# Kernel optimization log

Hardware: AMD Instinct MI355X
Metric: run time of the kernel (lower is better)

## Reference

```python
import jax, jax.numpy as jnp
import numpy as np

EPS_BN = 1e-5

def _l2n(v, axis):
    return v / jnp.maximum(jnp.linalg.norm(v, axis=axis, keepdims=True), 1e-12)

def _bn_relu(x, g, b):
    # x: [B, C, K]; BatchNorm2d training-mode stats over (B, K) per channel, then ReLU
    m = x.mean(axis=(0, 2), keepdims=True)
    v = x.var(axis=(0, 2), keepdims=True)
    return jax.nn.relu(g[None, :, None] * (x - m) * jax.lax.rsqrt(v + EPS_BN) + b[None, :, None])

def _conv_bn_relu(x, W, g, b):
    # 1x1 conv (no bias) == channel matmul
    return _bn_relu(jnp.einsum('oi,bik->bok', W, x), g, b)

def _graphnet(x, anchor, sigma_p):
    # NetVLAD-style soft assignment; vectorized over clusters (no [B,K,N,C] intermediate)
    B, C, H, W = x.shape
    N = H * W
    sig = jax.nn.sigmoid(sigma_p)                              # [K, C]
    xf = x.reshape(B, C, N).transpose(0, 2, 1)                 # [B, N, C]
    inv_s2 = 1.0 / (sig * sig)                                 # [K, C]
    q = (jnp.einsum('bnc,kc->bnk', xf * xf, inv_s2)
         - 2.0 * jnp.einsum('bnc,kc->bnk', xf, anchor * inv_s2)
         + jnp.sum(anchor * anchor * inv_s2, axis=-1))         # [B, N, K]
    assign = jax.nn.softmax(-0.5 * q.transpose(0, 2, 1), axis=1)  # [B, K, N], softmax over clusters
    s = assign.sum(axis=-1)                                    # [B, K]
    wx = jnp.einsum('bkn,bnc->bkc', assign, xf)                # [B, K, C]
    nodes = (wx - s[..., None] * anchor[None]) / sig[None] / (s[..., None] + 1e-9)
    nodes = _l2n(nodes, 2)
    flat = _l2n(nodes.reshape(B, -1), 1)
    # faithful to torch: flat view as (B, C, K) is a pure reshape of [B, K, C] data
    return flat.reshape(B, C, anchor.shape[0]), assign

def _cascade_gcn(x, W1, W2):
    # loop=2 cascaded GCN: adj = softmax(x^T x), out = (adj @ (x^T W))^T
    for Wg in (W1, W2):
        adj = jax.nn.softmax(jnp.einsum('bik,bil->bkl', x, x), axis=2)   # [B, K, K]
        sup = jnp.einsum('bik,io->bko', x, Wg)                           # [B, K, C]
        x = jnp.einsum('bkl,blo->bok', adj, sup)                         # [B, C, K]
    return jax.nn.relu(x)

def _mutual(edge, r1, r2, assign, g1, g2, cw, cg, cb):
    # cross-graph correlation + cascade GCN + project back to pixels
    a = jax.nn.softmax(jnp.einsum('bik,bil->bkl', edge, r1), axis=-1)    # [B, K, K]
    m = jnp.einsum('bkl,bcl->bck', a, r2)                                # [B, C, K]
    edge = _cascade_gcn(edge + m, g1, g2)
    ex = jnp.einsum('bck,bkn->bcn', edge, assign)                        # [B, C, N]
    return _conv_bn_relu(ex, cw, cg, cb)


def setup_inputs() -> dict:
    key = jax.random.key(0)
    B, C, H, W, K = 16, 256, 64, 64, 8
    ks = jax.random.split(key, 40)
    sc = 1.0 / np.sqrt(C)
    d = {
        'rgb':   jax.random.normal(ks[0], (B, C, H, W), jnp.float32),
        't':     jax.random.normal(ks[1], (B, C, H, W), jnp.float32),
        'edger': jax.random.normal(ks[2], (B, C, H, W), jnp.float32),
        'edget': jax.random.normal(ks[3], (B, C, H, W), jnp.float32),
        'pred_w': jax.random.normal(ks[4], (1, C), jnp.float32) * sc,
        'pred_b': jax.random.normal(ks[5], (1,), jnp.float32) * 0.1,
        'rgb_anchor': jax.random.uniform(ks[6], (K, C), jnp.float32),
        'rgb_sigma':  jax.random.uniform(ks[7], (K, C), jnp.float32),
        't_anchor':   jax.random.uniform(ks[8], (K, C), jnp.float32),
        't_sigma':    jax.random.uniform(ks[9], (K, C), jnp.float32),
    }
    i = 10
    for name in ['rgb_c1', 'rgb_c2', 't_c1', 't_c2', 't2r_conv', 'r2t_conv']:
        d[name + '_w'] = jax.random.normal(ks[i], (C, C), jnp.float32) * sc; i += 1
        d[name + '_g'] = jax.random.uniform(ks[i], (C,), jnp.float32); i += 1
        d[name + '_b'] = jnp.zeros((C,), jnp.float32)
    for name in ['t2r_g1', 't2r_g2', 'r2t_g1', 'r2t_g2']:
        d[name + '_w'] = jax.random.normal(ks[i], (C, C), jnp.float32) * sc; i += 1
    return d


def reference(rgb, t, edger, edget, pred_w, pred_b,
              rgb_anchor, rgb_sigma, t_anchor, t_sigma,
              rgb_c1_w, rgb_c1_g, rgb_c1_b, rgb_c2_w, rgb_c2_g, rgb_c2_b,
              t_c1_w, t_c1_g, t_c1_b, t_c2_w, t_c2_g, t_c2_b,
              t2r_conv_w, t2r_conv_g, t2r_conv_b,
              r2t_conv_w, r2t_conv_g, r2t_conv_b,
              t2r_g1_w, t2r_g2_w, r2t_g1_w, r2t_g2_w):
    # edge-gated features
    edge_r = jnp.einsum('oi,bihw->bohw', pred_w, edger) + pred_b.reshape(1, -1, 1, 1)
    rgb_x = jax.nn.sigmoid(edge_r) * rgb
    edge_t = jnp.einsum('oi,bihw->bohw', pred_w, edget) + pred_b.reshape(1, -1, 1, 1)
    t_x = jax.nn.sigmoid(edge_t) * t
    # graph projection
    rgb_graph, rgb_assign = _graphnet(rgb_x, rgb_anchor, rgb_sigma)
    t_graph, t_assign = _graphnet(t_x, t_anchor, t_sigma)
    rgb_g1 = _conv_bn_relu(rgb_graph, rgb_c1_w, rgb_c1_g, rgb_c1_b)
    rgb_g2 = _conv_bn_relu(rgb_graph, rgb_c2_w, rgb_c2_g, rgb_c2_b)
    t_g1 = _conv_bn_relu(t_graph, t_c1_w, t_c1_g, t_c1_b)
    t_g2 = _conv_bn_relu(t_graph, t_c2_w, t_c2_g, t_c2_b)
    # mutual graph interaction
    n_rgb = _mutual(rgb_graph, t_g1, t_g2, rgb_assign, t2r_g1_w, t2r_g2_w,
                    t2r_conv_w, t2r_conv_g, t2r_conv_b)
    rgb_x = rgb_x + n_rgb.reshape(rgb_x.shape)
    n_t = _mutual(t_graph, rgb_g1, rgb_g2, t_assign, r2t_g1_w, r2t_g2_w,
                  r2t_conv_w, r2t_conv_g, r2t_conv_b)
    t_x = t_x + n_t.reshape(t_x.shape)
    return (rgb_x, t_x)
```

## Files before the change

kernel.cpp:

```cpp
#include <hip/hip_runtime.h>
#include <math.h>

#define BB 16
#define CC 256
#define NN 4096
#define KK 8

#define OFF_S      ((size_t)0)
#define OFF_WX     ((size_t)256)
#define OFF_G      ((size_t)65792)
#define OFF_CS     ((size_t)67840)
#define OFF_MS     ((size_t)69888)
#define OFF_CK     ((size_t)70912)
#define ACC_FLOATS ((size_t)70928)
#define OFF_ASSIGN ((size_t)70928)
#define OFF_GRAPH  ((size_t)1119504)
#define OFF_CLP    ((size_t)1185040)
#define OFF_WT     ((size_t)1193232)
#define OFF_Y      ((size_t)1586448)
#define OFF_CE     ((size_t)1717520)
#define WS_FLOATS  ((size_t)1783056)

__global__ __launch_bounds__(256) void k0_prep(
    const float* __restrict__ w0, const float* __restrict__ w1,
    const float* __restrict__ w2, const float* __restrict__ w3,
    const float* __restrict__ w4, const float* __restrict__ w5,
    const float* __restrict__ anch_r, const float* __restrict__ sig_r,
    const float* __restrict__ anch_t, const float* __restrict__ sig_t,
    float* __restrict__ ws)
{
    int bid = blockIdx.x, tid = threadIdx.x;
    if (bid < 1536) {
        int widx = bid >> 8;
        int e = ((bid & 255) << 8) + tid;
        int o = e >> 8, i = e & 255;
        const float* W = widx == 0 ? w0 : widx == 1 ? w1 : widx == 2 ? w2 :
                         widx == 3 ? w3 : widx == 4 ? w4 : w5;
        ws[OFF_WT + (size_t)widx * 65536 + (size_t)i * 256 + o] = W[o * 256 + i];
    } else {
        int pid = ((bid - 1536) << 8) + tid;
        int M = pid >> 11, j = pid & 2047;
        int k = j >> 8, c = j & 255;
        const float* sg = M ? sig_t : sig_r;
        const float* an = M ? anch_t : anch_r;
        float s = 1.f / (1.f + expf(-sg[j]));
        float is2 = 1.f / (s * s);
        float a = an[j];
        float2* c2 = (float2*)(ws + OFF_CLP);
        c2[(size_t)M * 2048 + (size_t)c * 8 + k] = make_float2(is2, -2.f * a * is2);
        atomicAdd(&ws[OFF_CK + (size_t)M * 8 + k], a * a * is2);
    }
}

__global__ __launch_bounds__(256) void k1_gate_assign(
    const float* __restrict__ rgb, const float* __restrict__ t,
    const float* __restrict__ edger, const float* __restrict__ edget,
    const float* __restrict__ pred_w, const float* __restrict__ pred_b,
    float* __restrict__ out, float* __restrict__ ws)
{
    int tile = blockIdx.x;
    int b    = blockIdx.y;
    int M    = blockIdx.z;
    int tid  = threadIdx.x;
    int tx = tid & 63, ty = tid >> 6;
    int n0 = tile * 64;

    const float* X = M ? t : rgb;
    const float* E = M ? edget : edger;

    __shared__ _Float16 xs[CC][66];
    __shared__ float qp[KK][4][64];
    __shared__ float gatep[4][64];
    __shared__ float gate_s[64];
    __shared__ float asg[KK][64];
    __shared__ float cks[KK];

    if (tid < KK) cks[tid] = ws[OFF_CK + (size_t)M * 8 + tid];

    const float* Eb = E + ((size_t)b * CC) * NN + n0 + tx;
    float acc = 0.f;
#pragma unroll 4
    for (int c = ty * 64; c < ty * 64 + 64; ++c)
        acc += pred_w[c] * Eb[(size_t)c * NN];
    gatep[ty][tx] = acc;
    __syncthreads();
    if (tid < 64) {
        float g = gatep[0][tx] + gatep[1][tx] + gatep[2][tx] + gatep[3][tx] + pred_b[0];
        float sg = 1.f / (1.f + expf(-g));
        gate_s[tx] = sg;
        out[(((size_t)M * BB + b) * CC) * NN + n0 + tx] = sg;
    }
    __syncthreads();

    const float* Xb = X + ((size_t)b * CC) * NN + n0 + tx;
    const float4* prq = (const float4*)(ws + OFF_CLP) + (size_t)M * 1024;
    float gt = gate_s[tx];
    float qk[KK];
#pragma unroll
    for (int k = 0; k < KK; ++k) qk[k] = 0.f;
#pragma unroll 2
    for (int c = ty * 64; c < ty * 64 + 64; ++c) {
        float x = gt * Xb[(size_t)c * NN];
        xs[c][tx] = (_Float16)x;
        float xx = x * x;
        float4 p0 = prq[c * 4 + 0];
        float4 p1 = prq[c * 4 + 1];
        float4 p2 = prq[c * 4 + 2];
        float4 p3 = prq[c * 4 + 3];
        qk[0] += xx * p0.x + x * p0.y;  qk[1] += xx * p0.z + x * p0.w;
        qk[2] += xx * p1.x + x * p1.y;  qk[3] += xx * p1.z + x * p1.w;
        qk[4] += xx * p2.x + x * p2.y;  qk[5] += xx * p2.z + x * p2.w;
        qk[6] += xx * p3.x + x * p3.y;  qk[7] += xx * p3.z + x * p3.w;
    }
#pragma unroll
    for (int k = 0; k < KK; ++k) qp[k][ty][tx] = qk[k];
    __syncthreads();

    float* assign_g = ws + OFF_ASSIGN + (((size_t)M * BB + b) * KK) * NN;
    if (tid < 64) {
        float q[KK], mx = -1e30f;
#pragma unroll
        for (int k = 0; k < KK; ++k) {
            q[k] = -0.5f * (qp[k][0][tx] + qp[k][1][tx] + qp[k][2][tx] + qp[k][3][tx] + cks[k]);
            mx = fmaxf(mx, q[k]);
        }
        float sm = 0.f;
#pragma unroll
        for (int k = 0; k < KK; ++k) { q[k] = expf(q[k] - mx); sm += q[k]; }
        float inv = 1.f / sm;
#pragma unroll
        for (int k = 0; k < KK; ++k) {
            float a = q[k] * inv;
            asg[k][tx] = a;
            assign_g[(size_t)k * NN + n0 + tx] = a;
        }
    }
    __syncthreads();

    {
        int c = tid;
        float a0[KK];
#pragma unroll
        for (int k = 0; k < KK; ++k) a0[k] = 0.f;
#pragma unroll 4
        for (int j = 0; j < 64; ++j) {
            float xv = (float)xs[c][j];
#pragma unroll
            for (int k = 0; k < KK; ++k) a0[k] += asg[k][j] * xv;
        }
        float* wx_g = ws + OFF_WX + ((size_t)M * BB + b) * KK * CC;
#pragma unroll
        for (int k = 0; k < KK; ++k)
            atomicAdd(&wx_g[k * CC + c], a0[k]);
    }
    if (tid < 64) {
        int k1 = tid >> 3, k2 = tid & 7;
        float g = 0.f;
        for (int j = 0; j < 64; ++j) g += asg[k1][j] * asg[k2][j];
        atomicAdd(&ws[OFF_G + ((size_t)M * BB + b) * 64 + tid], g);
    } else if (tid < 72) {
        int k = tid - 64;
        float sv = 0.f;
        for (int j = 0; j < 64; ++j) sv += asg[k][j];
        atomicAdd(&ws[OFF_S + ((size_t)M * BB + b) * KK + k], sv);
    }
}

__global__ __launch_bounds__(256) void k2_nodes(
    const float* __restrict__ anch_r, const float* __restrict__ sig_r,
    const float* __restrict__ anch_t, const float* __restrict__ sig_t,
    float* __restrict__ ws)
{
    int b = blockIdx.x & 15, M = blockIdx.x >> 4;
    int c = threadIdx.x;
    const float* an = M ? anch_t : anch_r;
    const float* sg = M ? sig_t : sig_r;
    const float* wx = ws + OFF_WX + ((size_t)M * BB + b) * KK * CC;
    const float* sp = ws + OFF_S + ((size_t)M * BB + b) * KK;
    float* gout = ws + OFF_GRAPH + ((size_t)M * BB + b) * 2048;

    __shared__ float nod[KK][CC];
    __shared__ float nrm[KK];
    __shared__ float gp[CC];
    __shared__ float gnrm;

    float node[KK];
#pragma unroll
    for (int k = 0; k < KK; ++k) {
        float s = sp[k];
        float sig = 1.f / (1.f + expf(-sg[k * CC + c]));
        float v = (wx[k * CC + c] - s * an[k * CC + c]) / sig / (s + 1e-9f);
        node[k] = v;
        nod[k][c] = v;
    }
    __syncthreads();
    if (c < KK) {
        float ss = 0.f;
        for (int i = 0; i < CC; ++i) ss += nod[c][i] * nod[c][i];
        nrm[c] = fmaxf(sqrtf(ss), 1e-12f);
    }
    __syncthreads();
    float gs = 0.f;
#pragma unroll
    for (int k = 0; k < KK; ++k) { node[k] /= nrm[k]; gs += node[k] * node[k]; }
    gp[c] = gs;
    __syncthreads();
    if (c == 0) {
        float ss = 0.f;
        for (int i = 0; i < CC; ++i) ss += gp[i];
        gnrm = fmaxf(sqrtf(ss), 1e-12f);
    }
    __syncthreads();
    float inv = 1.f / gnrm;
#pragma unroll
    for (int k = 0; k < KK; ++k)
        gout[k * CC + c] = node[k] * inv;
}

__global__ __launch_bounds__(256) void k3_conv(float* __restrict__ ws)
{
    int conv = blockIdx.x >> 4, b = blockIdx.x & 15;
    int o = threadIdx.x;
    int M = conv >> 1;
    const float* gsrc = ws + OFF_GRAPH + ((size_t)M * BB + b) * 2048;
    const float* wt = ws + OFF_WT + (size_t)conv * 65536;
    __shared__ float gsh[2048];
    for (int i = o; i < 2048; i += 256) gsh[i] = gsrc[i];
    __syncthreads();
    float acc[KK];
#pragma unroll
    for (int k = 0; k < KK; ++k) acc[k] = 0.f;
    for (int i = 0; i < CC; ++i) {
        float w = wt[(size_t)i * 256 + o];
#pragma unroll
        for (int k = 0; k < KK; ++k) acc[k] += w * gsh[i * 8 + k];
    }
    float* y = ws + OFF_Y + ((size_t)conv * BB + b) * 2048;
    float s1 = 0.f, s2 = 0.f;
#pragma unroll
    for (int k = 0; k < KK; ++k) { y[o * 8 + k] = acc[k]; s1 += acc[k]; s2 += acc[k] * acc[k]; }
    atomicAdd(&ws[OFF_CS + (size_t)conv * 512 + o], s1);
    atomicAdd(&ws[OFF_CS + (size_t)conv * 512 + 256 + o], s2);
}

__device__ __forceinline__ void gcn_layer(const float* __restrict__ Wg,
                                          float* xin, float* xout, float* am,
                                          float* sup, int o, bool do_relu)
{
    if (o < 64) {
        int k = o >> 3, l = o & 7;
        float s = 0.f;
        for (int i = 0; i < CC; ++i) s += xin[i * 9 + k] * xin[i * 9 + l];
        am[k * 9 + l] = s;
    }
    __syncthreads();
    if (o < 8) {
        float mx = -1e30f;
#pragma unroll
        for (int l = 0; l < 8; ++l) mx = fmaxf(mx, am[o * 9 + l]);
        float e[8], sm = 0.f;
#pragma unroll
        for (int l = 0; l < 8; ++l) { e[l] = expf(am[o * 9 + l] - mx); sm += e[l]; }
        float inv = 1.f / sm;
#pragma unroll
        for (int l = 0; l < 8; ++l) am[o * 9 + l] = e[l] * inv;
    }
    float sa[8];
#pragma unroll
    for (int k = 0; k < 8; ++k) sa[k] = 0.f;
    for (int i = 0; i < CC; ++i) {
        float w = Wg[(size_t)i * 256 + o];
#pragma unroll
        for (int k = 0; k < 8; ++k) sa[k] += xin[i * 9 + k] * w;
    }
#pragma unroll
    for (int k = 0; k < 8; ++k) sup[k * 256 + o] = sa[k];
    __syncthreads();
#pragma unroll
    for (int k = 0; k < 8; ++k) {
        float v = 0.f;
#pragma unroll
        for (int l = 0; l < 8; ++l) v += am[k * 9 + l] * sup[l * 256 + o];
        xout[o * 9 + k] = do_relu ? fmaxf(v, 0.f) : v;
    }
    __syncthreads();
}

__global__ __launch_bounds__(256) void k4_mutual(
    const float* __restrict__ rc1g, const float* __restrict__ rc1b,
    const float* __restrict__ rc2g, const float* __restrict__ rc2b,
    const float* __restrict__ tc1g, const float* __restrict__ tc1b,
    const float* __restrict__ tc2g, const float* __restrict__ tc2b,
    const float* __restrict__ t2rg1, const float* __restrict__ t2rg2,
    const float* __restrict__ r2tg1, const float* __restrict__ r2tg2,
    float* __restrict__ ws)
{
    int D = blockIdx.x >> 4, b = blockIdx.x & 15;
    int o = threadIdx.x;
    int M = D;
    int convR1 = D ? 0 : 2;
    int convR2 = D ? 1 : 3;
    const float* g1p = D ? rc1g : tc1g;  const float* b1p = D ? rc1b : tc1b;
    const float* g2p = D ? rc2g : tc2g;  const float* b2p = D ? rc2b : tc2b;
    const float* gcn1 = D ? r2tg1 : t2rg1;
    const float* gcn2 = D ? r2tg2 : t2rg2;
    const float* cwT = ws + OFF_WT + (size_t)(4 + D) * 65536;

    __shared__ float edge_s[CC * 9];
    __shared__ float r1_s[CC * 9];
    __shared__ float r2_s[CC * 9];
    __shared__ float x0[CC * 9];
    __shared__ float x1[CC * 9];
    __shared__ float sup[KK * CC];
    __shared__ float am[KK * 9];
    __shared__ float sS[KK];
    __shared__ float gS[64];

    if (o < 8)  sS[o] = ws[OFF_S + ((size_t)M * BB + b) * 8 + o];
    if (o < 64) gS[o] = ws[OFF_G + ((size_t)M * BB + b) * 64 + o];

    const float* egr = ws + OFF_GRAPH + ((size_t)M * BB + b) * 2048;
    const float* y1 = ws + OFF_Y + ((size_t)convR1 * BB + b) * 2048;
    const float* y2 = ws + OFF_Y + ((size_t)convR2 * BB + b) * 2048;
    float m1 = ws[OFF_CS + (size_t)convR1 * 512 + o] * (1.f / 128.f);
    float q1 = ws[OFF_CS + (size_t)convR1 * 512 + 256 + o] * (1.f / 128.f);
    float al1 = g1p[o] * rsqrtf(q1 - m1 * m1 + 1e-5f);
    float be1 = b1p[o] - m1 * al1;
    float m2 = ws[OFF_CS + (size_t)convR2 * 512 + o] * (1.f / 128.f);
    float q2 = ws[OFF_CS + (size_t)convR2 * 512 + 256 + o] * (1.f / 128.f);
    float al2 = g2p[o] * rsqrtf(q2 - m2 * m2 + 1e-5f);
    float be2 = b2p[o] - m2 * al2;
#pragma unroll
    for (int k = 0; k < 8; ++k) {
        edge_s[o * 9 + k] = egr[o * 8 + k];
        r1_s[o * 9 + k] = fmaxf(al1 * y1[o * 8 + k] + be1, 0.f);
        r2_s[o * 9 + k] = fmaxf(al2 * y2[o * 8 + k] + be2, 0.f);
    }
    __syncthreads();

    if (o < 64) {
        int k = o >> 3, l = o & 7;
        float s = 0.f;
        for (int i = 0; i < CC; ++i) s += edge_s[i * 9 + k] * r1_s[i * 9 + l];
        am[k * 9 + l] = s;
    }
    __syncthreads();
    if (o < 8) {
        float mx = -1e30f;
#pragma unroll
        for (int l = 0; l < 8; ++l) mx = fmaxf(mx, am[o * 9 + l]);
        float e[8], sm = 0.f;
#pragma unroll
        for (int l = 0; l < 8; ++l) { e[l] = expf(am[o * 9 + l] - mx); sm += e[l]; }
        float inv = 1.f / sm;
#pragma unroll
        for (int l = 0; l < 8; ++l) am[o * 9 + l] = e[l] * inv;
    }
    __syncthreads();

#pragma unroll
    for (int k = 0; k < 8; ++k) {
        float mm = 0.f;
#pragma unroll
        for (int l = 0; l < 8; ++l) mm += am[k * 9 + l] * r2_s[o * 9 + l];
        x0[o * 9 + k] = edge_s[o * 9 + k] + mm;
    }
    __syncthreads();

    gcn_layer(gcn1, x0, x1, am, sup, o, false);
    gcn_layer(gcn2, x1, x0, am, sup, o, true);

    float ac[8];
#pragma unroll
    for (int k = 0; k < 8; ++k) ac[k] = 0.f;
    for (int i = 0; i < CC; ++i) {
        float w = cwT[(size_t)i * 256 + o];
#pragma unroll
        for (int k = 0; k < 8; ++k) ac[k] += w * x0[i * 9 + k];
    }
    float* ce = ws + OFF_CE + ((size_t)D * BB + b) * 2048;
    float smv = 0.f, sqv = 0.f;
#pragma unroll
    for (int k = 0; k < 8; ++k) {
        ce[o * 8 + k] = ac[k];
        smv += ac[k] * sS[k];
#pragma unroll
        for (int l = 0; l < 8; ++l) sqv += ac[k] * ac[l] * gS[k * 8 + l];
    }
    atomicAdd(&ws[OFF_MS + (size_t)D * 512 + o], smv);
    atomicAdd(&ws[OFF_MS + (size_t)D * 512 + 256 + o], sqv);
}

__global__ __launch_bounds__(512) void k6_final(
    const float* __restrict__ rgb, const float* __restrict__ t,
    const float* __restrict__ t2rg, const float* __restrict__ t2rb,
    const float* __restrict__ r2tg, const float* __restrict__ r2tb,
    float* __restrict__ out, const float* __restrict__ ws)
{
    int chunk = blockIdx.x;
    int b = blockIdx.y, D = blockIdx.z;
    int tid = threadIdx.x;
    int tn = tid & 255, th = tid >> 8;
    int n = chunk * 256 + tn;

    const float* X = D ? t : rgb;
    float* obase = out + (((size_t)D * BB + b) * CC) * NN;

    float gt = obase[n];

    const float* assign_g = ws + OFF_ASSIGN + (((size_t)D * BB + b) * KK) * NN;
    float a0 = assign_g[0 * NN + n], a1 = assign_g[1 * NN + n];
    float a2 = assign_g[2 * NN + n], a3 = assign_g[3 * NN + n];
    float a4 = assign_g[4 * NN + n], a5 = assign_g[5 * NN + n];
    float a6 = assign_g[6 * NN + n], a7 = assign_g[7 * NN + n];

    __shared__ __align__(16) float ce_s[2048];
    __shared__ float al_s[256], be_s[256];
    const float* ce = ws + OFF_CE + ((size_t)D * BB + b) * 2048;
    for (int i = tid; i < 2048; i += 512) ce_s[i] = ce[i];
    if (tid < 256) {
        int o = tid;
        float m = ws[OFF_MS + (size_t)D * 512 + o] * (1.f / 65536.f);
        float q = ws[OFF_MS + (size_t)D * 512 + 256 + o] * (1.f / 65536.f);
        const float* g = D ? r2tg : t2rg;
        const float* bb = D ? r2tb : t2rb;
        float al = g[o] * rsqrtf(q - m * m + 1e-5f);
        al_s[o] = al;
        be_s[o] = bb[o] - m * al;
    }
    __syncthreads();

    const float* Xb = X + ((size_t)b * CC) * NN + n;
    const float4* ce4 = (const float4*)ce_s;
#pragma unroll 4
    for (int i = 0; i < 128; ++i) {
        int c = th * 128 + i;
        float4 ca = ce4[2 * c];
        float4 cb = ce4[2 * c + 1];
        float y = ca.x * a0 + ca.y * a1 + ca.z * a2 + ca.w * a3
                + cb.x * a4 + cb.y * a5 + cb.z * a6 + cb.w * a7;
        float v = fmaxf(al_s[c] * y + be_s[c], 0.f);
        obase[(size_t)c * NN + n] = gt * Xb[(size_t)c * NN] + v;
    }
}

extern "C" void kernel_launch(void* const* d_in, const int* in_sizes, int n_in,
                              void* d_out, int out_size, void* d_ws, size_t ws_size,
                              hipStream_t stream) {
    (void)in_sizes; (void)n_in; (void)out_size; (void)ws_size;
    const float* rgb    = (const float*)d_in[0];
    const float* t      = (const float*)d_in[1];
    const float* edger  = (const float*)d_in[2];
    const float* edget  = (const float*)d_in[3];
    const float* pred_w = (const float*)d_in[4];
    const float* pred_b = (const float*)d_in[5];
    const float* anch_r = (const float*)d_in[6];
    const float* sig_r  = (const float*)d_in[7];
    const float* anch_t = (const float*)d_in[8];
    const float* sig_t  = (const float*)d_in[9];
    const float* rc1w = (const float*)d_in[10];
    const float* rc1g = (const float*)d_in[11];
    const float* rc1b = (const float*)d_in[12];
    const float* rc2w = (const float*)d_in[13];
    const float* rc2g = (const float*)d_in[14];
    const float* rc2b = (const float*)d_in[15];
    const float* tc1w = (const float*)d_in[16];
    const float* tc1g = (const float*)d_in[17];
    const float* tc1b = (const float*)d_in[18];
    const float* tc2w = (const float*)d_in[19];
    const float* tc2g = (const float*)d_in[20];
    const float* tc2b = (const float*)d_in[21];
    const float* t2rcw = (const float*)d_in[22];
    const float* t2rcg = (const float*)d_in[23];
    const float* t2rcb = (const float*)d_in[24];
    const float* r2tcw = (const float*)d_in[25];
    const float* r2tcg = (const float*)d_in[26];
    const float* r2tcb = (const float*)d_in[27];
    const float* t2rg1 = (const float*)d_in[28];
    const float* t2rg2 = (const float*)d_in[29];
    const float* r2tg1 = (const float*)d_in[30];
    const float* r2tg2 = (const float*)d_in[31];

    float* out = (float*)d_out;
    float* ws = (float*)d_ws;

    hipMemsetAsync(ws, 0, ACC_FLOATS * sizeof(float), stream);
    k0_prep<<<1552, 256, 0, stream>>>(rc1w, rc2w, tc1w, tc2w, t2rcw, r2tcw,
                                      anch_r, sig_r, anch_t, sig_t, ws);
    k1_gate_assign<<<dim3(64, 16, 2), 256, 0, stream>>>(rgb, t, edger, edget,
                                                        pred_w, pred_b, out, ws);
    k2_nodes<<<32, 256, 0, stream>>>(anch_r, sig_r, anch_t, sig_t, ws);
    k3_conv<<<64, 256, 0, stream>>>(ws);
    k4_mutual<<<32, 256, 0, stream>>>(rc1g, rc1b, rc2g, rc2b, tc1g, tc1b, tc2g, tc2b,
                                      t2rg1, t2rg2, r2tg1, r2tg2, ws);
    k6_final<<<dim3(16, 16, 2), 512, 0, stream>>>(rgb, t, t2rcg, t2rcb, r2tcg, r2tcb,
                                                  out, ws);
}
```

Baseline: 626.8 us.

## Split edge gate into its own kernel, stage cluster params in LDS, vectorize final pass

Moves the edge-gate channel reduction out of the assignment kernel into a separate kernel that reads float2 per thread and writes the gate to the output buffer. The assignment kernel then reads the gate back from global memory and keeps the per-cluster parameters in shared memory instead of re-reading them from global memory for every channel. The final kernel now handles two pixels per thread with float2 loads and stores, halving the per-thread channel loop. This adds a kernel launch, and the gate kernel uses only 256 blocks, so it may underfill the GPU while it streams the edge tensors.

```diff
diff --git a/kernel.cpp b/kernel.cpp
--- a/kernel.cpp
+++ b/kernel.cpp
@@ -52,11 +52,33 @@
     }
 }
 
-__global__ __launch_bounds__(256) void k1_gate_assign(
-    const float* __restrict__ rgb, const float* __restrict__ t,
+__global__ __launch_bounds__(256) void kgate(
     const float* __restrict__ edger, const float* __restrict__ edget,
     const float* __restrict__ pred_w, const float* __restrict__ pred_b,
-    float* __restrict__ out, float* __restrict__ ws)
+    float* __restrict__ out)
+{
+    int chunk = blockIdx.x;
+    int b = blockIdx.y, M = blockIdx.z;
+    int n = chunk * 512 + threadIdx.x * 2;
+    const float* E = M ? edget : edger;
+    const float* Eb = E + ((size_t)b * CC) * NN + n;
+    float ax = 0.f, ay = 0.f;
+#pragma unroll 8
+    for (int c = 0; c < CC; ++c) {
+        float w = pred_w[c];
+        float2 e = *(const float2*)(Eb + (size_t)c * NN);
+        ax += w * e.x; ay += w * e.y;
+    }
+    float pb = pred_b[0];
+    float2 g;
+    g.x = 1.f / (1.f + expf(-(ax + pb)));
+    g.y = 1.f / (1.f + expf(-(ay + pb)));
+    *(float2*)(out + (((size_t)M * BB + b) * CC) * NN + n) = g;
+}
+
+__global__ __launch_bounds__(256) void k1_assign(
+    const float* __restrict__ rgb, const float* __restrict__ t,
+    const float* __restrict__ out, float* __restrict__ ws)
 {
     int tile = blockIdx.x;
     int b    = blockIdx.y;
@@ -66,47 +88,33 @@
     int n0 = tile * 64;
 
     const float* X = M ? t : rgb;
-    const float* E = M ? edget : edger;
 
     __shared__ _Float16 xs[CC][66];
+    __shared__ float4 pr4[1024];
     __shared__ float qp[KK][4][64];
-    __shared__ float gatep[4][64];
-    __shared__ float gate_s[64];
     __shared__ float asg[KK][64];
     __shared__ float cks[KK];
 
+    const float4* prg = (const float4*)(ws + OFF_CLP) + (size_t)M * 1024;
+    for (int i = tid; i < 1024; i += 256) pr4[i] = prg[i];
     if (tid < KK) cks[tid] = ws[OFF_CK + (size_t)M * 8 + tid];
 
-    const float* Eb = E + ((size_t)b * CC) * NN + n0 + tx;
-    float acc = 0.f;
+    float gt = out[(((size_t)M * BB + b) * CC) * NN + n0 + tx];
+    __syncthreads();
+
+    const float* Xb = X + ((size_t)b * CC) * NN + n0 + tx;
+    float qk[KK];
+#pragma unroll
+    for (int k = 0; k < KK; ++k) qk[k] = 0.f;
 #pragma unroll 4
-    for (int c = ty * 64; c < ty * 64 + 64; ++c)
-        acc += pred_w[c] * Eb[(size_t)c * NN];
-    gatep[ty][tx] = acc;
-    __syncthreads();
-    if (tid < 64) {
-        float g = gatep[0][tx] + gatep[1][tx] + gatep[2][tx] + gatep[3][tx] + pred_b[0];
-        float sg = 1.f / (1.f + expf(-g));
-        gate_s[tx] = sg;
-        out[(((size_t)M * BB + b) * CC) * NN + n0 + tx] = sg;
-    }
-    __syncthreads();
-
-    const float* Xb = X + ((size_t)b * CC) * NN + n0 + tx;
-    const float4* prq = (const float4*)(ws + OFF_CLP) + (size_t)M * 1024;
-    float gt = gate_s[tx];
-    float qk[KK];
-#pragma unroll
-    for (int k = 0; k < KK; ++k) qk[k] = 0.f;
-#pragma unroll 2
     for (int c = ty * 64; c < ty * 64 + 64; ++c) {
         float x = gt * Xb[(size_t)c * NN];
         xs[c][tx] = (_Float16)x;
         float xx = x * x;
-        float4 p0 = prq[c * 4 + 0];
-        float4 p1 = prq[c * 4 + 1];
-        float4 p2 = prq[c * 4 + 2];
-        float4 p3 = prq[c * 4 + 3];
+        float4 p0 = pr4[c * 4 + 0];
+        float4 p1 = pr4[c * 4 + 1];
+        float4 p2 = pr4[c * 4 + 2];
+        float4 p3 = pr4[c * 4 + 3];
         qk[0] += xx * p0.x + x * p0.y;  qk[1] += xx * p0.z + x * p0.w;
         qk[2] += xx * p1.x + x * p1.y;  qk[3] += xx * p1.z + x * p1.w;
         qk[4] += xx * p2.x + x * p2.y;  qk[5] += xx * p2.z + x * p2.w;
@@ -400,24 +408,25 @@
     int chunk = blockIdx.x;
     int b = blockIdx.y, D = blockIdx.z;
     int tid = threadIdx.x;
-    int tn = tid & 255, th = tid >> 8;
-    int n = chunk * 256 + tn;
+    int ln = tid & 127;
+    int th = tid >> 7;
+    int n = chunk * 256 + ln * 2;
 
     const float* X = D ? t : rgb;
     float* obase = out + (((size_t)D * BB + b) * CC) * NN;
 
-    float gt = obase[n];
+    float2 gt2 = *(const float2*)(obase + n);
 
     const float* assign_g = ws + OFF_ASSIGN + (((size_t)D * BB + b) * KK) * NN;
-    float a0 = assign_g[0 * NN + n], a1 = assign_g[1 * NN + n];
-    float a2 = assign_g[2 * NN + n], a3 = assign_g[3 * NN + n];
-    float a4 = assign_g[4 * NN + n], a5 = assign_g[5 * NN + n];
-    float a6 = assign_g[6 * NN + n], a7 = assign_g[7 * NN + n];
-
-    __shared__ __align__(16) float ce_s[2048];
+    float2 a[KK];
+#pragma unroll
+    for (int k = 0; k < KK; ++k)
+        a[k] = *(const float2*)(assign_g + (size_t)k * NN + n);
+
+    __shared__ __align__(16) float4 ce_s[512];
     __shared__ float al_s[256], be_s[256];
-    const float* ce = ws + OFF_CE + ((size_t)D * BB + b) * 2048;
-    for (int i = tid; i < 2048; i += 512) ce_s[i] = ce[i];
+    const float4* ce = (const float4*)(ws + OFF_CE + ((size_t)D * BB + b) * 2048);
+    ce_s[tid] = ce[tid];
     if (tid < 256) {
         int o = tid;
         float m = ws[OFF_MS + (size_t)D * 512 + o] * (1.f / 65536.f);
@@ -431,16 +440,21 @@
     __syncthreads();
 
     const float* Xb = X + ((size_t)b * CC) * NN + n;
-    const float4* ce4 = (const float4*)ce_s;
 #pragma unroll 4
-    for (int i = 0; i < 128; ++i) {
-        int c = th * 128 + i;
-        float4 ca = ce4[2 * c];
-        float4 cb = ce4[2 * c + 1];
-        float y = ca.x * a0 + ca.y * a1 + ca.z * a2 + ca.w * a3
-                + cb.x * a4 + cb.y * a5 + cb.z * a6 + cb.w * a7;
-        float v = fmaxf(al_s[c] * y + be_s[c], 0.f);
-        obase[(size_t)c * NN + n] = gt * Xb[(size_t)c * NN] + v;
+    for (int i = 0; i < 64; ++i) {
+        int c = th * 64 + i;
+        float4 ca = ce_s[2 * c];
+        float4 cb = ce_s[2 * c + 1];
+        float2 xv = *(const float2*)(Xb + (size_t)c * NN);
+        float y0 = ca.x * a[0].x + ca.y * a[1].x + ca.z * a[2].x + ca.w * a[3].x
+                 + cb.x * a[4].x + cb.y * a[5].x + cb.z * a[6].x + cb.w * a[7].x;
+        float y1 = ca.x * a[0].y + ca.y * a[1].y + ca.z * a[2].y + ca.w * a[3].y
+                 + cb.x * a[4].y + cb.y * a[5].y + cb.z * a[6].y + cb.w * a[7].y;
+        float al = al_s[c], be = be_s[c];
+        float2 r;
+        r.x = gt2.x * xv.x + fmaxf(al * y0 + be, 0.f);
+        r.y = gt2.y * xv.y + fmaxf(al * y1 + be, 0.f);
+        *(float2*)(obase + (size_t)c * NN + n) = r;
     }
 }
 
@@ -487,8 +501,8 @@
     hipMemsetAsync(ws, 0, ACC_FLOATS * sizeof(float), stream);
     k0_prep<<<1552, 256, 0, stream>>>(rc1w, rc2w, tc1w, tc2w, t2rcw, r2tcw,
                                       anch_r, sig_r, anch_t, sig_t, ws);
-    k1_gate_assign<<<dim3(64, 16, 2), 256, 0, stream>>>(rgb, t, edger, edget,
-                                                        pred_w, pred_b, out, ws);
+    kgate<<<dim3(8, 16, 2), 256, 0, stream>>>(edger, edget, pred_w, pred_b, out);
+    k1_assign<<<dim3(64, 16, 2), 256, 0, stream>>>(rgb, t, out, ws);
     k2_nodes<<<32, 256, 0, stream>>>(anch_r, sig_r, anch_t, sig_t, ws);
     k3_conv<<<64, 256, 0, stream>>>(ws);
     k4_mutual<<<32, 256, 0, stream>>>(rc1g, rc1b, rc2g, rc2b, tc1g, tc1b, tc2g, tc2b,
```

After: 591.7 us. 1.06x faster.
